# Kernel optimization log

Hardware: AMD Instinct MI355X
Metric: run time of the kernel (lower is better)

## Reference

```python
import jax, jax.numpy as jnp
import numpy as np

IMAGE_SIZE = 128
PATCH_SIZE = 8
BOND_DIM = 128
CP_RANK = 64
EMBED_DIM = 512
BATCH = 512
GRID = IMAGE_SIZE // PATCH_SIZE            # 16
NUM_PATCHES = GRID * GRID                  # 256
DEPTH = 4                                  # log4(256)
LEVEL_NODES = [64, 16, 4, 1]


def setup_inputs() -> dict:
    key = jax.random.key(0)
    ks = jax.random.split(key, 32)
    s = 0.02
    inp = {
        "x": jax.random.normal(ks[0], (BATCH, 1, IMAGE_SIZE, IMAGE_SIZE), jnp.float32),
        "W_patch": jax.random.normal(ks[1], (PATCH_SIZE * PATCH_SIZE, BOND_DIM), jnp.float32) * s,
        "b_patch": jnp.zeros((BOND_DIM,), jnp.float32),
        "pos": jax.random.normal(ks[2], (1, NUM_PATCHES, BOND_DIM), jnp.float32),
        "gamma": jnp.ones((BOND_DIM,), jnp.float32),
        "beta": jnp.zeros((BOND_DIM,), jnp.float32),
        "W_head": jax.random.normal(ks[3], (BOND_DIM, EMBED_DIM), jnp.float32) * s,
        "b_head": jnp.zeros((EMBED_DIM,), jnp.float32),
    }
    for lvl, n in enumerate(LEVEL_NODES):
        # per-node distinct CP factors: 4 children in_dim->rank, then rank->out_dim
        inp[f"f{lvl}"] = jax.random.normal(ks[4 + 2 * lvl], (n, 4, BOND_DIM, CP_RANK), jnp.float32) * s
        inp[f"o{lvl}"] = jax.random.normal(ks[5 + 2 * lvl], (n, CP_RANK, BOND_DIM), jnp.float32) * s
    return inp


def _patchify(x):
    # 'b c (h p1) (w p2) -> b (h w) (p1 p2 c)', c == 1
    b = x.shape[0]
    x = x.reshape(b, 1, GRID, PATCH_SIZE, GRID, PATCH_SIZE)
    x = x.transpose(0, 2, 4, 3, 5, 1)                  # b h w p1 p2 c
    return x.reshape(b, NUM_PATCHES, PATCH_SIZE * PATCH_SIZE)


def _quad_group(x, grid):
    # 'b (h w) c -> b (h/2 w/2) (h2 w2) c' with 2x2 blocks
    b, _, c = x.shape
    g2 = grid // 2
    x = x.reshape(b, g2, 2, g2, 2, c).transpose(0, 1, 3, 2, 4, 5)
    return x.reshape(b, g2 * g2, 4, c)


def _cp_level(x, f, o):
    # x: [b, n, 4, C]; f: [n, 4, C, R]; o: [n, R, C]
    u = jnp.einsum('bnqc,nqcr->bnqr', x, f)
    p = jnp.prod(u, axis=2)                            # [b, n, R]
    return jnp.einsum('bnr,nrc->bnc', p, o)


def reference(x, W_patch, b_patch, pos, f0, o0, f1, o1, f2, o2, f3, o3,
              gamma, beta, W_head, b_head):
    h = _patchify(x) @ W_patch + b_patch               # [b, 256, C]
    h = h + pos
    grid = GRID
    for f, o in ((f0, o0), (f1, o1), (f2, o2), (f3, o3)):
        h = _cp_level(_quad_group(h, grid), f, o)
        grid //= 2
    h = h[:, 0, :]                                     # squeeze node dim
    mu = jnp.mean(h, axis=-1, keepdims=True)
    var = jnp.var(h, axis=-1, keepdims=True)
    h = (h - mu) / jnp.sqrt(var + 1e-5) * gamma + beta
    out = h @ W_head + b_head
    n = jnp.maximum(jnp.linalg.norm(out, axis=-1, keepdims=True), 1e-12)
    return out / n
```

## Files before the change

kernel.cpp:

```cpp
#include <hip/hip_runtime.h>
#include <hip/hip_bf16.h>

#define BATCH     512
#define IMG       128
#define PS        8
#define GRID_P    16
#define NP        256
#define C         128
#define R         64
#define E         512

typedef float f32x4 __attribute__((ext_vector_type(4)));
typedef short s16x8 __attribute__((ext_vector_type(8)));

__device__ __forceinline__ unsigned short f2bf(float x) {
    unsigned int u = __float_as_uint(x);
    u += 0x7fffu + ((u >> 16) & 1u);
    return (unsigned short)(u >> 16);
}
__device__ __forceinline__ float bf2f(unsigned short h) {
    return __uint_as_float(((unsigned int)h) << 16);
}

__global__ __launch_bounds__(256) void prep_all_kernel(
    const float* __restrict__ f0, const float* __restrict__ f1,
    const float* __restrict__ f2, const float* __restrict__ f3,
    const float* __restrict__ o0, const float* __restrict__ o1,
    const float* __restrict__ o2, const float* __restrict__ o3,
    const float* __restrict__ Wh, const float* __restrict__ Wp,
    const float* __restrict__ pos, const float* __restrict__ bp,
    unsigned short* __restrict__ fTL, unsigned short* __restrict__ oT,
    unsigned short* __restrict__ WhT, unsigned short* __restrict__ WfT,
    float* __restrict__ pf)
{
    __shared__ float ls[128 * 68];
    __shared__ float red[64 * 4];
    const int bi = blockIdx.x, t = threadIdx.x;

    if (bi < 256) {
        const float* src = f0 + (size_t)bi * 8192;
#pragma unroll
        for (int i = 0; i < 8; ++i) {
            const int fi = (t + 256 * i) * 4;
            const int c = fi >> 6, r = fi & 63;
            *(float4*)(ls + c * 68 + r) = *(const float4*)(src + fi);
        }
        __syncthreads();

        const int w = t >> 6, lane = t & 63;
        const int m = lane & 15, g = lane >> 4;

        f32x4 acc[4];
#pragma unroll
        for (int nt = 0; nt < 4; ++nt) acc[nt] = (f32x4){0.f, 0.f, 0.f, 0.f};
#pragma unroll
        for (int kt = 0; kt < 4; ++kt) {
            s16x8 afr;
#pragma unroll
            for (int e = 0; e < 8; ++e)
                afr[e] = (short)f2bf(ls[(kt * 32 + g * 8 + e) * 68 + w * 16 + m]);
#pragma unroll
            for (int nt = 0; nt < 4; ++nt) {
                const float* wr = Wp + (size_t)(nt * 16 + m) * 128 + kt * 32 + g * 8;
                const float4 b0 = *(const float4*)wr;
                const float4 b1 = *(const float4*)(wr + 4);
                s16x8 bfr;
                bfr[0] = (short)f2bf(b0.x); bfr[1] = (short)f2bf(b0.y);
                bfr[2] = (short)f2bf(b0.z); bfr[3] = (short)f2bf(b0.w);
                bfr[4] = (short)f2bf(b1.x); bfr[5] = (short)f2bf(b1.y);
                bfr[6] = (short)f2bf(b1.z); bfr[7] = (short)f2bf(b1.w);
                acc[nt] = __builtin_amdgcn_mfma_f32_16x16x32_bf16(afr, bfr, acc[nt], 0, 0, 0);
            }
        }
        unsigned short* D = WfT + (size_t)bi * 4096;
#pragma unroll
        for (int nt = 0; nt < 4; ++nt)
#pragma unroll
            for (int j = 0; j < 4; ++j)
                D[(size_t)(w * 16 + g * 4 + j) * 64 + nt * 16 + m] = f2bf(acc[nt][j]);

        {
            const int r = t & 63, half = t >> 6;
            const int n0 = bi >> 2, q = bi & 3;
            const int pp = (2 * (n0 >> 3) + (q >> 1)) * GRID_P + 2 * (n0 & 7) + (q & 1);
            const float* posr = pos + (size_t)pp * C;
            float s = 0.f;
#pragma unroll 8
            for (int e = 0; e < 32; ++e) {
                const int c = half * 32 + e;
                s += (posr[c] + bp[c]) * ls[c * 68 + r];
            }
            red[r * 4 + half] = s;
        }
        __syncthreads();
        if (t < 64)
            pf[bi * 64 + t] = red[t * 4 + 0] + red[t * 4 + 1] + red[t * 4 + 2] + red[t * 4 + 3];
    } else if (bi < 340) {
        const int ti = bi - 256;
        const float* src;
        if      (ti < 64) src = f1 + (size_t)ti * 8192;
        else if (ti < 80) src = f2 + (size_t)(ti - 64) * 8192;
        else              src = f3 + (size_t)(ti - 80) * 8192;
        unsigned short* dst = fTL + (size_t)ti * 8192;
#pragma unroll
        for (int i = 0; i < 8; ++i) {
            const int fi = (t + 256 * i) * 4;
            const int c = fi >> 6, r = fi & 63;
            *(float4*)(ls + c * 68 + r) = *(const float4*)(src + fi);
        }
        __syncthreads();
        const int rr = t >> 2, seg = t & 3;
        unsigned int* d32 = (unsigned int*)(dst + rr * 128 + seg * 32);
#pragma unroll
        for (int ii = 0; ii < 16; ++ii) {
            const int c = seg * 32 + ii * 2;
            const unsigned int lo = f2bf(ls[c * 68 + rr]);
            const unsigned int hi = f2bf(ls[(c + 1) * 68 + rr]);
            d32[ii] = lo | (hi << 16);
        }
    } else if (bi < 425) {
        const int oi = bi - 340;
        const float* src;
        if      (oi < 64) src = o0 + (size_t)oi * 8192;
        else if (oi < 80) src = o1 + (size_t)(oi - 64) * 8192;
        else if (oi < 84) src = o2 + (size_t)(oi - 80) * 8192;
        else              src = o3 + (size_t)(oi - 84) * 8192;
        unsigned short* dst = oT + (size_t)oi * 8192;
#pragma unroll
        for (int i = 0; i < 8; ++i) {
            const int fi = (t + 256 * i) * 4;
            const int r = fi >> 7, c = fi & 127;
            *(float4*)(ls + r * 132 + c) = *(const float4*)(src + fi);
        }
        __syncthreads();
        const int cc = t >> 1, seg = t & 1;
        unsigned int* d32 = (unsigned int*)(dst + cc * 64 + seg * 32);
#pragma unroll
        for (int ii = 0; ii < 16; ++ii) {
            const int r = seg * 32 + ii * 2;
            const unsigned int lo = f2bf(ls[r * 132 + cc]);
            const unsigned int hi = f2bf(ls[(r + 1) * 132 + cc]);
            d32[ii] = lo | (hi << 16);
        }
    } else {
        const int j = bi - 425;
#pragma unroll
        for (int i = 0; i < 8; ++i) {
            const int fi = (t + 256 * i) * 4;
            const int c = fi >> 6, e = fi & 63;
            *(float4*)(ls + c * 68 + e) = *(const float4*)(Wh + (size_t)c * E + j * 64 + e);
        }
        __syncthreads();
        const int rr = t >> 2, seg = t & 3;
        unsigned int* d32 = (unsigned int*)(WhT + (size_t)(j * 64 + rr) * 128 + seg * 32);
#pragma unroll
        for (int ii = 0; ii < 16; ++ii) {
            const int c = seg * 32 + ii * 2;
            const unsigned int lo = f2bf(ls[c * 68 + rr]);
            const unsigned int hi = f2bf(ls[(c + 1) * 68 + rr]);
            d32[ii] = lo | (hi << 16);
        }
    }
}

__global__ __launch_bounds__(256) void level01_fused(
    const float* __restrict__ x,
    const unsigned short* __restrict__ WfT,
    const float* __restrict__ pf,
    const unsigned short* __restrict__ oT,
    const unsigned short* __restrict__ fT1,
    unsigned short* __restrict__ h2)
{
    __shared__ __align__(16) unsigned short pixs[16 * 1026];
    __shared__ __align__(16) float          us1[4 * 16 * 68];
    __shared__ __align__(16) unsigned short ps0[4 * 16 * 72];
    __shared__ __align__(16) unsigned short ps1[16 * 72];
    __shared__ __align__(16) unsigned short h1s[4 * 16 * 136];

    const int bi = blockIdx.x;
    const int n1 = bi >> 5, btile = bi & 31;
    const int t = threadIdx.x, w = t >> 6, lane = t & 63;
    const int m = lane & 15, g = lane >> 4;
    const int bt = btile * 16;

    const int y1g = n1 >> 2, x1g = n1 & 3;
    const int Ry0 = y1g * 32, Rx0 = x1g * 32;
    const int n0 = (2 * y1g + (w >> 1)) * 8 + 2 * x1g + (w & 1);

#pragma unroll
    for (int i = 0; i < 16; ++i) {
        const int idx = i * 256 + t;
        const int c4 = idx & 7, rowg = (idx >> 3) & 31, bl = idx >> 8;
        const float4 p4 = *(const float4*)(x + ((size_t)(bt + bl) * IMG + Ry0 + rowg) * IMG + Rx0 + c4 * 4);
        uint2 v;
        v.x = (unsigned int)f2bf(p4.x) | ((unsigned int)f2bf(p4.y) << 16);
        v.y = (unsigned int)f2bf(p4.z) | ((unsigned int)f2bf(p4.w) << 16);
        *(uint2*)(pixs + bl * 1026 + rowg * 32 + c4 * 4) = v;
    }
    __syncthreads();

    s16x8 a[4][2];
    {
        const int rbase = 16 * (w >> 1);
        const int cbase = 16 * (w & 1);
#pragma unroll
        for (int q = 0; q < 4; ++q) {
            const int rq = rbase + 8 * (q >> 1) + g;
            const int cc = cbase + 8 * (q & 1);
#pragma unroll
            for (int kt = 0; kt < 2; ++kt)
                a[q][kt] = *(const s16x8*)(pixs + m * 1026 + (rq + kt * 4) * 32 + cc);
        }
    }

    f32x4 accu[4][4];
#pragma unroll
    for (int q = 0; q < 4; ++q) {
        const float* pfq = pf + (size_t)(n0 * 4 + q) * 64;
#pragma unroll
        for (int nt = 0; nt < 4; ++nt) {
            const float pv = pfq[nt * 16 + m];
            accu[q][nt] = (f32x4){pv, pv, pv, pv};
        }
    }
#pragma unroll
    for (int q = 0; q < 4; ++q) {
        const unsigned short* Wq = WfT + (size_t)(n0 * 4 + q) * 4096;
#pragma unroll
        for (int kt = 0; kt < 2; ++kt) {
            const int koff = kt * 32 + g * 8;
#pragma unroll
            for (int nt = 0; nt < 4; ++nt) {
                const s16x8 bfr = *(const s16x8*)(Wq + (size_t)(nt * 16 + m) * 64 + koff);
                accu[q][nt] = __builtin_amdgcn_mfma_f32_16x16x32_bf16(a[q][kt], bfr, accu[q][nt], 0, 0, 0);
            }
        }
    }

    unsigned short* myps = ps0 + w * (16 * 72);
#pragma unroll
    for (int nt = 0; nt < 4; ++nt) {
        const f32x4 pr = accu[0][nt] * accu[1][nt] * accu[2][nt] * accu[3][nt];
#pragma unroll
        for (int j = 0; j < 4; ++j)
            myps[(g * 4 + j) * 72 + nt * 16 + m] = f2bf(pr[j]);
    }

    {
        s16x8 ap[2];
#pragma unroll
        for (int kt = 0; kt < 2; ++kt)
            ap[kt] = *(const s16x8*)(myps + m * 72 + kt * 32 + g * 8);
        const unsigned short* oTn = oT + (size_t)n0 * 8192;
        unsigned short* myh = h1s + w * (16 * 136);
#pragma unroll
        for (int ct = 0; ct < 8; ++ct) {
            f32x4 aco = (f32x4){0.f, 0.f, 0.f, 0.f};
#pragma unroll
            for (int kt = 0; kt < 2; ++kt) {
                const s16x8 bfr = *(const s16x8*)(oTn + (size_t)(ct * 16 + m) * 64 + kt * 32 + g * 8);
                aco = __builtin_amdgcn_mfma_f32_16x16x32_bf16(ap[kt], bfr, aco, 0, 0, 0);
            }
#pragma unroll
            for (int j = 0; j < 4; ++j)
                myh[(g * 4 + j) * 136 + ct * 16 + m] = f2bf(aco[j]);
        }
    }

    {
        const unsigned short* myh = h1s + w * (16 * 136);
        const unsigned short* fq = fT1 + (size_t)(n1 * 4 + w) * 8192;
        f32x4 au[4];
#pragma unroll
        for (int nt = 0; nt < 4; ++nt) au[nt] = (f32x4){0.f, 0.f, 0.f, 0.f};
#pragma unroll
        for (int kt = 0; kt < 4; ++kt) {
            const int koff = kt * 32 + g * 8;
            const s16x8 afr = *(const s16x8*)(myh + m * 136 + koff);
#pragma unroll
            for (int nt = 0; nt < 4; ++nt) {
                const s16x8 bfr = *(const s16x8*)(fq + (size_t)(nt * 16 + m) * 128 + koff);
                au[nt] = __builtin_amdgcn_mfma_f32_16x16x32_bf16(afr, bfr, au[nt], 0, 0, 0);
            }
        }
#pragma unroll
        for (int nt = 0; nt < 4; ++nt)
#pragma unroll
            for (int j = 0; j < 4; ++j)
                us1[(w * 16 + g * 4 + j) * 68 + nt * 16 + m] = au[nt][j];
    }
    __syncthreads();

    {
        const int pb = t >> 4, r0 = (t & 15) * 4;
        const f32x4 u0 = *(const f32x4*)(us1 + (0 * 16 + pb) * 68 + r0);
        const f32x4 u1 = *(const f32x4*)(us1 + (1 * 16 + pb) * 68 + r0);
        const f32x4 u2 = *(const f32x4*)(us1 + (2 * 16 + pb) * 68 + r0);
        const f32x4 u3 = *(const f32x4*)(us1 + (3 * 16 + pb) * 68 + r0);
        const f32x4 p = u0 * u1 * u2 * u3;
        uint2 v;
        v.x = (unsigned int)f2bf(p[0]) | ((unsigned int)f2bf(p[1]) << 16);
        v.y = (unsigned int)f2bf(p[2]) | ((unsigned int)f2bf(p[3]) << 16);
        *(uint2*)(ps1 + pb * 72 + r0) = v;
    }
    __syncthreads();

    {
        s16x8 ap[2];
#pragma unroll
        for (int kt = 0; kt < 2; ++kt)
            ap[kt] = *(const s16x8*)(ps1 + m * 72 + kt * 32 + g * 8);
        const unsigned short* oTn = oT + (size_t)(64 + n1) * 8192;
#pragma unroll
        for (int i = 0; i < 2; ++i) {
            const int ct = w * 2 + i;
            f32x4 aco = (f32x4){0.f, 0.f, 0.f, 0.f};
#pragma unroll
            for (int kt = 0; kt < 2; ++kt) {
                const s16x8 bfr = *(const s16x8*)(oTn + (size_t)(ct * 16 + m) * 64 + kt * 32 + g * 8);
                aco = __builtin_amdgcn_mfma_f32_16x16x32_bf16(ap[kt], bfr, aco, 0, 0, 0);
            }
#pragma unroll
            for (int j = 0; j < 4; ++j)
                h2[((size_t)(bt + g * 4 + j) * 16 + n1) * C + ct * 16 + m] = f2bf(aco[j]);
        }
    }
}

__global__ __launch_bounds__(256) void tail_kernel(
    const unsigned short* __restrict__ h2,
    const unsigned short* __restrict__ fT2,
    const unsigned short* __restrict__ oT2,
    const unsigned short* __restrict__ fT3,
    const unsigned short* __restrict__ oT3,
    const float* __restrict__ gamma, const float* __restrict__ beta,
    const unsigned short* __restrict__ WhT,
    const float* __restrict__ bh,
    float* __restrict__ out)
{
    __shared__ __align__(16) float          us3[4 * 16 * 68];
    __shared__ __align__(16) unsigned short ps2[4 * 16 * 72];
    __shared__ __align__(16) unsigned short ps3[16 * 72];
    __shared__ __align__(16) unsigned short h3s[16 * 4 * 136];
    __shared__ __align__(16) float          h4s[16 * 132];
    __shared__ __align__(16) unsigned short hns[16 * 136];
    __shared__ float red[16 * 4];

    const int bt = blockIdx.x * 16;
    const int t = threadIdx.x, w = t >> 6, lane = t & 63;
    const int m = lane & 15, g = lane >> 4;

    {
        const int n2 = w;
        const int y1 = n2 >> 1, x1 = n2 & 1;
        f32x4 acc_u[4][4];
#pragma unroll
        for (int q = 0; q < 4; ++q)
#pragma unroll
            for (int nt = 0; nt < 4; ++nt) acc_u[q][nt] = (f32x4){0.f, 0.f, 0.f, 0.f};
#pragma unroll
        for (int q = 0; q < 4; ++q) {
            const int pidx = (2 * y1 + (q >> 1)) * 4 + 2 * x1 + (q & 1);
            const unsigned short* xq = h2 + ((size_t)(bt + m) * 16 + pidx) * C;
            const unsigned short* fq = fT2 + (size_t)(n2 * 4 + q) * R * C;
#pragma unroll
            for (int kt = 0; kt < 4; ++kt) {
                const int koff = kt * 32 + g * 8;
                const s16x8 a = *(const s16x8*)(xq + koff);
#pragma unroll
                for (int nt = 0; nt < 4; ++nt) {
                    const s16x8 bfr = *(const s16x8*)(fq + (size_t)(nt * 16 + m) * C + koff);
                    acc_u[q][nt] = __builtin_amdgcn_mfma_f32_16x16x32_bf16(a, bfr, acc_u[q][nt], 0, 0, 0);
                }
            }
        }
        unsigned short* myps = ps2 + w * 16 * 72;
#pragma unroll
        for (int nt = 0; nt < 4; ++nt) {
            const f32x4 p = acc_u[0][nt] * acc_u[1][nt] * acc_u[2][nt] * acc_u[3][nt];
#pragma unroll
            for (int j = 0; j < 4; ++j)
                myps[(g * 4 + j) * 72 + nt * 16 + m] = f2bf(p[j]);
        }
        f32x4 aco[8];
#pragma unroll
        for (int ct = 0; ct < 8; ++ct) aco[ct] = (f32x4){0.f, 0.f, 0.f, 0.f};
        const unsigned short* oTn = oT2 + (size_t)n2 * C * R;
#pragma unroll
        for (int kt = 0; kt < 2; ++kt) {
            const int koff = kt * 32 + g * 8;
            const s16x8 a = *(const s16x8*)(myps + m * 72 + koff);
#pragma unroll
            for (int ct = 0; ct < 8; ++ct) {
                const s16x8 bfr = *(const s16x8*)(oTn + (size_t)(ct * 16 + m) * R + koff);
                aco[ct] = __builtin_amdgcn_mfma_f32_16x16x32_bf16(a, bfr, aco[ct], 0, 0, 0);
            }
        }
#pragma unroll
        for (int ct = 0; ct < 8; ++ct)
#pragma unroll
            for (int j = 0; j < 4; ++j)
                h3s[((g * 4 + j) * 4 + n2) * 136 + ct * 16 + m] = f2bf(aco[ct][j]);
    }
    __syncthreads();

    {
        const int q = w;
        const unsigned short* fq = fT3 + (size_t)q * R * C;
        f32x4 acc_u[4];
#pragma unroll
        for (int nt = 0; nt < 4; ++nt) acc_u[nt] = (f32x4){0.f, 0.f, 0.f, 0.f};
#pragma unroll
        for (int kt = 0; kt < 4; ++kt) {
            const int koff = kt * 32 + g * 8;
            const s16x8 a = *(const s16x8*)(h3s + (m * 4 + q) * 136 + koff);
#pragma unroll
            for (int nt = 0; nt < 4; ++nt) {
                const s16x8 bfr = *(const s16x8*)(fq + (size_t)(nt * 16 + m) * C + koff);
                acc_u[nt] = __builtin_amdgcn_mfma_f32_16x16x32_bf16(a, bfr, acc_u[nt], 0, 0, 0);
            }
        }
#pragma unroll
        for (int nt = 0; nt < 4; ++nt)
#pragma unroll
            for (int j = 0; j < 4; ++j)
                us3[(q * 16 + g * 4 + j) * 68 + nt * 16 + m] = acc_u[nt][j];
    }
    __syncthreads();
    {
        const int pb = t >> 4, r0 = (t & 15) * 4;
        const f32x4 u0 = *(const f32x4*)(us3 + (0 * 16 + pb) * 68 + r0);
        const f32x4 u1 = *(const f32x4*)(us3 + (1 * 16 + pb) * 68 + r0);
        const f32x4 u2 = *(const f32x4*)(us3 + (2 * 16 + pb) * 68 + r0);
        const f32x4 u3 = *(const f32x4*)(us3 + (3 * 16 + pb) * 68 + r0);
        const f32x4 p = u0 * u1 * u2 * u3;
        uint2 v;
        v.x = (unsigned int)f2bf(p[0]) | ((unsigned int)f2bf(p[1]) << 16);
        v.y = (unsigned int)f2bf(p[2]) | ((unsigned int)f2bf(p[3]) << 16);
        *(uint2*)(ps3 + pb * 72 + r0) = v;
    }
    __syncthreads();
    {
        s16x8 ap[2];
#pragma unroll
        for (int kt = 0; kt < 2; ++kt)
            ap[kt] = *(const s16x8*)(ps3 + m * 72 + kt * 32 + g * 8);
#pragma unroll
        for (int i = 0; i < 2; ++i) {
            f32x4 aco = (f32x4){0.f, 0.f, 0.f, 0.f};
            const int ct = w * 2 + i;
#pragma unroll
            for (int kt = 0; kt < 2; ++kt) {
                const s16x8 bfr = *(const s16x8*)(oT3 + (size_t)(ct * 16 + m) * R + kt * 32 + g * 8);
                aco = __builtin_amdgcn_mfma_f32_16x16x32_bf16(ap[kt], bfr, aco, 0, 0, 0);
            }
#pragma unroll
            for (int j = 0; j < 4; ++j)
                h4s[(g * 4 + j) * 132 + ct * 16 + m] = aco[j];
        }
    }
    __syncthreads();

    {
        const int rb = w * 4 + g;
        const int c0 = m * 8;
        const f32x4 v0 = *(const f32x4*)(h4s + rb * 132 + c0);
        const f32x4 v1 = *(const f32x4*)(h4s + rb * 132 + c0 + 4);
        float s  = v0[0] + v0[1] + v0[2] + v0[3] + v1[0] + v1[1] + v1[2] + v1[3];
        float ss = v0[0]*v0[0] + v0[1]*v0[1] + v0[2]*v0[2] + v0[3]*v0[3]
                 + v1[0]*v1[0] + v1[1]*v1[1] + v1[2]*v1[2] + v1[3]*v1[3];
#pragma unroll
        for (int off = 1; off < 16; off <<= 1) {
            s  += __shfl_xor(s, off);
            ss += __shfl_xor(ss, off);
        }
        const float mu   = s * (1.f / C);
        const float var  = ss * (1.f / C) - mu * mu;
        const float rstd = rsqrtf(var + 1e-5f);
        const f32x4 ga0 = *(const f32x4*)(gamma + c0);
        const f32x4 ga1 = *(const f32x4*)(gamma + c0 + 4);
        const f32x4 be0 = *(const f32x4*)(beta + c0);
        const f32x4 be1 = *(const f32x4*)(beta + c0 + 4);
        unsigned int o32[4];
        float hv[8];
#pragma unroll
        for (int k = 0; k < 4; ++k) hv[k]     = (v0[k] - mu) * rstd * ga0[k] + be0[k];
#pragma unroll
        for (int k = 0; k < 4; ++k) hv[4 + k] = (v1[k] - mu) * rstd * ga1[k] + be1[k];
#pragma unroll
        for (int k = 0; k < 4; ++k)
            o32[k] = (unsigned int)f2bf(hv[2*k]) | ((unsigned int)f2bf(hv[2*k+1]) << 16);
        *(uint4*)(hns + rb * 136 + c0) = *(uint4*)o32;
    }
    __syncthreads();

    {
        f32x4 acc[8];
#pragma unroll
        for (int nt = 0; nt < 8; ++nt) {
            const int e = w * 128 + nt * 16 + m;
            const float bv = bh[e];
            acc[nt] = (f32x4){bv, bv, bv, bv};
        }
#pragma unroll
        for (int kt = 0; kt < 4; ++kt) {
            const int koff = kt * 32 + g * 8;
            const s16x8 a = *(const s16x8*)(hns + m * 136 + koff);
#pragma unroll
            for (int nt = 0; nt < 8; ++nt) {
                const int e = w * 128 + nt * 16 + m;
                const s16x8 bfr = *(const s16x8*)(WhT + (size_t)e * 128 + koff);
                acc[nt] = __builtin_amdgcn_mfma_f32_16x16x32_bf16(a, bfr, acc[nt], 0, 0, 0);
            }
        }
        float sq[4];
#pragma unroll
        for (int j = 0; j < 4; ++j) {
            float s = 0.f;
#pragma unroll
            for (int nt = 0; nt < 8; ++nt) s += acc[nt][j] * acc[nt][j];
#pragma unroll
            for (int off = 1; off < 16; off <<= 1) s += __shfl_xor(s, off);
            sq[j] = s;
        }
        if (m == 0) {
#pragma unroll
            for (int j = 0; j < 4; ++j) red[(g * 4 + j) * 4 + w] = sq[j];
        }
        __syncthreads();
#pragma unroll
        for (int j = 0; j < 4; ++j) {
            const int row = g * 4 + j;
            const float tot = red[row * 4 + 0] + red[row * 4 + 1]
                            + red[row * 4 + 2] + red[row * 4 + 3];
            const float inv = 1.f / fmaxf(sqrtf(tot), 1e-12f);
#pragma unroll
            for (int nt = 0; nt < 8; ++nt) {
                const int e = w * 128 + nt * 16 + m;
                out[(size_t)(bt + row) * E + e] = acc[nt][j] * inv;
            }
        }
    }
}

extern "C" void kernel_launch(void* const* d_in, const int* in_sizes, int n_in,
                              void* d_out, int out_size, void* d_ws, size_t ws_size,
                              hipStream_t stream) {
    const float* x     = (const float*)d_in[0];
    const float* Wp    = (const float*)d_in[1];
    const float* bp    = (const float*)d_in[2];
    const float* pos   = (const float*)d_in[3];
    const float* gamma = (const float*)d_in[4];
    const float* beta  = (const float*)d_in[5];
    const float* Wh    = (const float*)d_in[6];
    const float* bh    = (const float*)d_in[7];
    const float* f0    = (const float*)d_in[8];
    const float* o0    = (const float*)d_in[9];
    const float* f1    = (const float*)d_in[10];
    const float* o1    = (const float*)d_in[11];
    const float* f2    = (const float*)d_in[12];
    const float* o2    = (const float*)d_in[13];
    const float* f3    = (const float*)d_in[14];
    const float* o3    = (const float*)d_in[15];
    float* out = (float*)d_out;

    unsigned short* h2  = (unsigned short*)d_ws;
    unsigned short* fTL = h2 + (size_t)1048576;
    unsigned short* oT  = fTL + (size_t)688128;
    unsigned short* WfT = oT + (size_t)696320;
    unsigned short* WhT = WfT + (size_t)1048576;
    float*          pff = (float*)(WhT + 65536);

    unsigned short* fT1 = fTL;
    unsigned short* fT2 = fTL + (size_t)64 * 8192;
    unsigned short* fT3 = fTL + (size_t)80 * 8192;
    unsigned short* oT2 = oT + (size_t)80 * 8192;
    unsigned short* oT3 = oT + (size_t)84 * 8192;

    prep_all_kernel<<<433, 256, 0, stream>>>(f0, f1, f2, f3, o0, o1, o2, o3,
                                             Wh, Wp, pos, bp,
                                             fTL, oT, WhT, WfT, pff);

    level01_fused<<<16 * 32, 256, 0, stream>>>(x, WfT, pff, oT, fT1, h2);

    tail_kernel<<<32, 256, 0, stream>>>(h2, fT2, oT2, fT3, oT3,
                                        gamma, beta, WhT, bh, out);
}
```

Measured before the change: 152.0 us.

## Fuse tail kernel into level01 via last-block-done atomic counter per batch tile

Merges the tail kernel into the level-0/1 kernel. A per-batch-tile atomic counter, reset in the prep kernel, lets the last of the 16 node blocks for a tile carry on into levels 2-3, layernorm and the head. Shared memory is aliased between the two phases so the fused kernel's footprint stays bounded. This removes one kernel launch and the gap between kernels, at the cost of running the tail serially on whichever block finishes last, plus the atomic and fence overhead.

```diff
diff --git a/kernel.cpp b/kernel.cpp
--- a/kernel.cpp
+++ b/kernel.cpp
@@ -31,13 +31,14 @@
     const float* __restrict__ pos, const float* __restrict__ bp,
     unsigned short* __restrict__ fTL, unsigned short* __restrict__ oT,
     unsigned short* __restrict__ WhT, unsigned short* __restrict__ WfT,
-    float* __restrict__ pf)
+    float* __restrict__ pf, unsigned int* __restrict__ cnt)
 {
     __shared__ float ls[128 * 68];
     __shared__ float red[64 * 4];
     const int bi = blockIdx.x, t = threadIdx.x;
 
     if (bi < 256) {
+        if (bi == 0 && t < 32) cnt[t] = 0u;
         const float* src = f0 + (size_t)bi * 8192;
 #pragma unroll
         for (int i = 0; i < 8; ++i) {
@@ -163,19 +164,37 @@
     }
 }
 
-__global__ __launch_bounds__(256) void level01_fused(
+__global__ __launch_bounds__(256) void level01_tail_fused(
     const float* __restrict__ x,
     const unsigned short* __restrict__ WfT,
     const float* __restrict__ pf,
     const unsigned short* __restrict__ oT,
     const unsigned short* __restrict__ fT1,
-    unsigned short* __restrict__ h2)
+    unsigned short* __restrict__ h2,
+    unsigned int* __restrict__ cnt,
+    const unsigned short* __restrict__ fT2,
+    const unsigned short* __restrict__ oT2,
+    const unsigned short* __restrict__ fT3,
+    const unsigned short* __restrict__ oT3,
+    const float* __restrict__ gamma, const float* __restrict__ beta,
+    const unsigned short* __restrict__ WhT,
+    const float* __restrict__ bh,
+    float* __restrict__ out)
 {
-    __shared__ __align__(16) unsigned short pixs[16 * 1026];
-    __shared__ __align__(16) float          us1[4 * 16 * 68];
-    __shared__ __align__(16) unsigned short ps0[4 * 16 * 72];
-    __shared__ __align__(16) unsigned short ps1[16 * 72];
-    __shared__ __align__(16) unsigned short h1s[4 * 16 * 136];
+    __shared__ __align__(16) char smem[79168];
+    __shared__ unsigned int tail_go;
+    unsigned short* pixs = (unsigned short*)(smem);
+    float*          us1  = (float*)         (smem + 32832);
+    unsigned short* ps0  = (unsigned short*)(smem + 50240);
+    unsigned short* ps1  = (unsigned short*)(smem + 59456);
+    unsigned short* h1s  = (unsigned short*)(smem + 61760);
+    float*          us3  = (float*)         (smem);
+    unsigned short* ps2  = (unsigned short*)(smem + 17408);
+    unsigned short* ps3  = (unsigned short*)(smem + 26624);
+    unsigned short* h3s  = (unsigned short*)(smem + 28928);
+    float*          h4s  = (float*)         (smem + 46336);
+    unsigned short* hns  = (unsigned short*)(smem + 54784);
+    float*          redt = (float*)         (smem + 59136);
 
     const int bi = blockIdx.x;
     const int n1 = bi >> 5, btile = bi & 31;
@@ -325,30 +344,17 @@
                 h2[((size_t)(bt + g * 4 + j) * 16 + n1) * C + ct * 16 + m] = f2bf(aco[j]);
         }
     }
-}
-
-__global__ __launch_bounds__(256) void tail_kernel(
-    const unsigned short* __restrict__ h2,
-    const unsigned short* __restrict__ fT2,
-    const unsigned short* __restrict__ oT2,
-    const unsigned short* __restrict__ fT3,
-    const unsigned short* __restrict__ oT3,
-    const float* __restrict__ gamma, const float* __restrict__ beta,
-    const unsigned short* __restrict__ WhT,
-    const float* __restrict__ bh,
-    float* __restrict__ out)
-{
-    __shared__ __align__(16) float          us3[4 * 16 * 68];
-    __shared__ __align__(16) unsigned short ps2[4 * 16 * 72];
-    __shared__ __align__(16) unsigned short ps3[16 * 72];
-    __shared__ __align__(16) unsigned short h3s[16 * 4 * 136];
-    __shared__ __align__(16) float          h4s[16 * 132];
-    __shared__ __align__(16) unsigned short hns[16 * 136];
-    __shared__ float red[16 * 4];
-
-    const int bt = blockIdx.x * 16;
-    const int t = threadIdx.x, w = t >> 6, lane = t & 63;
-    const int m = lane & 15, g = lane >> 4;
+
+    __syncthreads();
+    if (t == 0) {
+        const unsigned int old =
+            __hip_atomic_fetch_add(&cnt[btile], 1u, __ATOMIC_ACQ_REL,
+                                   __HIP_MEMORY_SCOPE_AGENT);
+        tail_go = (old == 15u) ? 1u : 0u;
+    }
+    __syncthreads();
+    if (tail_go == 0u) return;
+    __builtin_amdgcn_fence(__ATOMIC_ACQUIRE, "agent");
 
     {
         const int n2 = w;
@@ -366,21 +372,21 @@
 #pragma unroll
             for (int kt = 0; kt < 4; ++kt) {
                 const int koff = kt * 32 + g * 8;
-                const s16x8 a = *(const s16x8*)(xq + koff);
+                const s16x8 av = *(const s16x8*)(xq + koff);
 #pragma unroll
                 for (int nt = 0; nt < 4; ++nt) {
                     const s16x8 bfr = *(const s16x8*)(fq + (size_t)(nt * 16 + m) * C + koff);
-                    acc_u[q][nt] = __builtin_amdgcn_mfma_f32_16x16x32_bf16(a, bfr, acc_u[q][nt], 0, 0, 0);
+                    acc_u[q][nt] = __builtin_amdgcn_mfma_f32_16x16x32_bf16(av, bfr, acc_u[q][nt], 0, 0, 0);
                 }
             }
         }
-        unsigned short* myps = ps2 + w * 16 * 72;
+        unsigned short* myps2 = ps2 + w * 16 * 72;
 #pragma unroll
         for (int nt = 0; nt < 4; ++nt) {
             const f32x4 p = acc_u[0][nt] * acc_u[1][nt] * acc_u[2][nt] * acc_u[3][nt];
 #pragma unroll
             for (int j = 0; j < 4; ++j)
-                myps[(g * 4 + j) * 72 + nt * 16 + m] = f2bf(p[j]);
+                myps2[(g * 4 + j) * 72 + nt * 16 + m] = f2bf(p[j]);
         }
         f32x4 aco[8];
 #pragma unroll
@@ -389,11 +395,11 @@
 #pragma unroll
         for (int kt = 0; kt < 2; ++kt) {
             const int koff = kt * 32 + g * 8;
-            const s16x8 a = *(const s16x8*)(myps + m * 72 + koff);
+            const s16x8 av = *(const s16x8*)(myps2 + m * 72 + koff);
 #pragma unroll
             for (int ct = 0; ct < 8; ++ct) {
                 const s16x8 bfr = *(const s16x8*)(oTn + (size_t)(ct * 16 + m) * R + koff);
-                aco[ct] = __builtin_amdgcn_mfma_f32_16x16x32_bf16(a, bfr, aco[ct], 0, 0, 0);
+                aco[ct] = __builtin_amdgcn_mfma_f32_16x16x32_bf16(av, bfr, aco[ct], 0, 0, 0);
             }
         }
 #pragma unroll
@@ -413,11 +419,11 @@
 #pragma unroll
         for (int kt = 0; kt < 4; ++kt) {
             const int koff = kt * 32 + g * 8;
-            const s16x8 a = *(const s16x8*)(h3s + (m * 4 + q) * 136 + koff);
+            const s16x8 av = *(const s16x8*)(h3s + (m * 4 + q) * 136 + koff);
 #pragma unroll
             for (int nt = 0; nt < 4; ++nt) {
                 const s16x8 bfr = *(const s16x8*)(fq + (size_t)(nt * 16 + m) * C + koff);
-                acc_u[nt] = __builtin_amdgcn_mfma_f32_16x16x32_bf16(a, bfr, acc_u[nt], 0, 0, 0);
+                acc_u[nt] = __builtin_amdgcn_mfma_f32_16x16x32_bf16(av, bfr, acc_u[nt], 0, 0, 0);
             }
         }
 #pragma unroll
@@ -505,12 +511,12 @@
 #pragma unroll
         for (int kt = 0; kt < 4; ++kt) {
             const int koff = kt * 32 + g * 8;
-            const s16x8 a = *(const s16x8*)(hns + m * 136 + koff);
+            const s16x8 av = *(const s16x8*)(hns + m * 136 + koff);
 #pragma unroll
             for (int nt = 0; nt < 8; ++nt) {
                 const int e = w * 128 + nt * 16 + m;
                 const s16x8 bfr = *(const s16x8*)(WhT + (size_t)e * 128 + koff);
-                acc[nt] = __builtin_amdgcn_mfma_f32_16x16x32_bf16(a, bfr, acc[nt], 0, 0, 0);
+                acc[nt] = __builtin_amdgcn_mfma_f32_16x16x32_bf16(av, bfr, acc[nt], 0, 0, 0);
             }
         }
         float sq[4];
@@ -525,14 +531,14 @@
         }
         if (m == 0) {
 #pragma unroll
-            for (int j = 0; j < 4; ++j) red[(g * 4 + j) * 4 + w] = sq[j];
+            for (int j = 0; j < 4; ++j) redt[(g * 4 + j) * 4 + w] = sq[j];
         }
         __syncthreads();
 #pragma unroll
         for (int j = 0; j < 4; ++j) {
             const int row = g * 4 + j;
-            const float tot = red[row * 4 + 0] + red[row * 4 + 1]
-                            + red[row * 4 + 2] + red[row * 4 + 3];
+            const float tot = redt[row * 4 + 0] + redt[row * 4 + 1]
+                            + redt[row * 4 + 2] + redt[row * 4 + 3];
             const float inv = 1.f / fmaxf(sqrtf(tot), 1e-12f);
 #pragma unroll
             for (int nt = 0; nt < 8; ++nt) {
@@ -570,6 +576,7 @@
     unsigned short* WfT = oT + (size_t)696320;
     unsigned short* WhT = WfT + (size_t)1048576;
     float*          pff = (float*)(WhT + 65536);
+    unsigned int*   cnt = (unsigned int*)(pff + 16384);
 
     unsigned short* fT1 = fTL;
     unsigned short* fT2 = fTL + (size_t)64 * 8192;
@@ -579,10 +586,9 @@
 
     prep_all_kernel<<<433, 256, 0, stream>>>(f0, f1, f2, f3, o0, o1, o2, o3,
                                              Wh, Wp, pos, bp,
-                                             fTL, oT, WhT, WfT, pff);
-
-    level01_fused<<<16 * 32, 256, 0, stream>>>(x, WfT, pff, oT, fT1, h2);
-
-    tail_kernel<<<32, 256, 0, stream>>>(h2, fT2, oT2, fT3, oT3,
-                                        gamma, beta, WhT, bh, out);
+                                             fTL, oT, WhT, WfT, pff, cnt);
+
+    level01_tail_fused<<<16 * 32, 256, 0, stream>>>(x, WfT, pff, oT, fT1, h2, cnt,
+                                                    fT2, oT2, fT3, oT3,
+                                                    gamma, beta, WhT, bh, out);
 }
```

Measured after the change: 166.3 us. 9.4% more time.
